# Optimization experiments

Measured on AMD Instinct MI355X. Metric: run time of the kernel, lower is better.

Reference implementation:

```python
import jax, jax.numpy as jnp
import numpy as np

N_NODES = 80000
N_EDGES = 1280000
IN_C, HID_C, OUT_C = 128, 64, 40


def setup_inputs() -> dict:
    key = jax.random.key(0)
    k1, k2, k3, k4 = jax.random.split(key, 4)
    x = jax.random.normal(k1, (N_NODES, IN_C), dtype=jnp.float32)
    edge_index = jax.random.randint(k2, (2, N_EDGES), 0, N_NODES, dtype=jnp.int32)
    W1 = jax.random.normal(k3, (IN_C, HID_C), dtype=jnp.float32) * (1.0 / np.sqrt(IN_C))
    W2 = jax.random.normal(k4, (HID_C, OUT_C), dtype=jnp.float32) * (1.0 / np.sqrt(HID_C))
    return {"x": x, "edge_index": edge_index, "W1": W1, "W2": W2}


def _spmm_add(edge_index, h):
    # adj_t.matmul(h): out[dst] += h[src]  (aggr='add', message = x_j)
    src, dst = edge_index[0], edge_index[1]
    return jax.ops.segment_sum(h[src], dst, num_segments=N_NODES)


def reference(x, edge_index, W1, W2):
    # GCNConv 1: linear (no bias) then add-aggregate SpMM
    h = _spmm_add(edge_index, x @ W1)          # [N, HID]
    h = jax.nn.relu(h)
    # GCNConv 2
    h = _spmm_add(edge_index, h @ W2)          # [N, OUT]
    return jax.nn.log_softmax(h, axis=-1)
```

## Files before the change

### kernel.cpp

```cpp
#include <hip/hip_runtime.h>
#include <hip/hip_bf16.h>
#include <math.h>

#define N_NODES 80000
#define N_EDGES 1280000
#define IN_C 128
#define HID_C 64
#define OUT_C 40

#define KB 313
#define BK_CAP 4600
#define EPT_A 8
#define NBLK_A 313
#define NBLK_G1 625

__device__ __forceinline__ float bf_lo(unsigned u) {
    union { unsigned i; float f; } c; c.i = u << 16; return c.f;
}
__device__ __forceinline__ float bf_hi(unsigned u) {
    union { unsigned i; float f; } c; c.i = u & 0xffff0000u; return c.f;
}
__device__ __forceinline__ unsigned pack_bf2(float a, float b) {
    union { float f; unsigned i; } ca, cb; ca.f = a; cb.f = b;
    unsigned ra = (ca.i + 0x7fffu + ((ca.i >> 16) & 1u)) >> 16;
    unsigned rb = (cb.i + 0x7fffu + ((cb.i >> 16) & 1u)) >> 16;
    return ra | (rb << 16);
}

typedef short v8s __attribute__((ext_vector_type(8)));
typedef float v4f __attribute__((ext_vector_type(4)));
typedef float v2f __attribute__((ext_vector_type(2)));
union U16 { uint4 u; v8s s; };

__device__ __forceinline__ v2f bf2f(unsigned u) {
    return (v2f){bf_lo(u), bf_hi(u)};
}

__global__ void prep_w_kernel(const float* __restrict__ W1, const float* __restrict__ W2,
                              unsigned* __restrict__ w1t, unsigned* __restrict__ w2t,
                              int* __restrict__ bcnt) {
    const int g = blockIdx.x * 256 + threadIdx.x;
    if (g < KB) bcnt[g] = 0;
    {
        const int wcol = g >> 6, kk = g & 63;
        w1t[g] = pack_bf2(W1[(2 * kk) * HID_C + wcol], W1[(2 * kk + 1) * HID_C + wcol]);
    }
    if (g < 1536) {
        const int wcol = g >> 5, kk = g & 31;
        w2t[g] = (wcol < OUT_C)
            ? pack_bf2(W2[(2 * kk) * OUT_C + wcol], W2[(2 * kk + 1) * OUT_C + wcol])
            : 0u;
    }
}

__global__ __launch_bounds__(512) void binA_gemm1_kernel(const int* __restrict__ src,
                                                         const int* __restrict__ dst,
                                                         int* __restrict__ bcnt,
                                                         int* __restrict__ gbuf,
                                                         const float* __restrict__ x,
                                                         const unsigned* __restrict__ w1t,
                                                         unsigned* __restrict__ h1b) {
    if (blockIdx.x >= NBLK_A) {
        const int tid = threadIdx.x;
        const int wave = tid >> 6, lane = tid & 63;
        const int nl = lane & 15, quad = lane >> 4;
        const int node = ((blockIdx.x - NBLK_A) * 8 + wave) * 16 + nl;

        v4f acc[4];
#pragma unroll
        for (int q = 0; q < 4; ++q) acc[q] = (v4f){0.f, 0.f, 0.f, 0.f};

#pragma unroll
        for (int kit = 0; kit < 4; ++kit) {
            const float* xp = x + (size_t)node * IN_C + kit * 32 + quad * 8;
            const float4 lo = *(const float4*)xp;
            const float4 hi = *(const float4*)(xp + 4);
            U16 bu;
            bu.u.x = pack_bf2(lo.x, lo.y); bu.u.y = pack_bf2(lo.z, lo.w);
            bu.u.z = pack_bf2(hi.x, hi.y); bu.u.w = pack_bf2(hi.z, hi.w);
#pragma unroll
            for (int mt = 0; mt < 4; ++mt) {
                U16 au;
                au.u = *(const uint4*)(w1t + ((mt * 16 + nl) * 64 + kit * 16 + quad * 4));
                acc[mt] = __builtin_amdgcn_mfma_f32_16x16x32_bf16(au.s, bu.s, acc[mt], 0, 0, 0);
            }
        }
#pragma unroll
        for (int mt = 0; mt < 4; ++mt) {
            uint2 o;
            o.x = pack_bf2(acc[mt][0], acc[mt][1]);
            o.y = pack_bf2(acc[mt][2], acc[mt][3]);
            *(uint2*)(h1b + (size_t)node * 32 + mt * 8 + quad * 2) = o;
        }
        return;
    }

    __shared__ int lcnt[KB];
    __shared__ int lexcl[KB];
    __shared__ int lbase[KB];
    __shared__ int lcur[KB];
    __shared__ int stage[512 * EPT_A];
    __shared__ int gaddr[512 * EPT_A];
    const int tid = threadIdx.x;

    for (int i = tid; i < KB; i += 512) lcnt[i] = 0;
    __syncthreads();

    const int e0 = blockIdx.x * 512 * EPT_A;
    int my_s[EPT_A], my_b[EPT_A], my_dl[EPT_A];
#pragma unroll
    for (int j = 0; j < EPT_A; ++j) {
        const int e = e0 + j * 512 + tid;
        if (e < N_EDGES) {
            const int d = dst[e];
            my_s[j] = src[e];
            my_b[j] = d >> 8;
            my_dl[j] = d & 255;
            atomicAdd(&lcnt[my_b[j]], 1);
        } else my_b[j] = -1;
    }
    __syncthreads();

    if (tid < KB) lexcl[tid] = lcnt[tid];
    __syncthreads();
    for (int o = 1; o < KB; o <<= 1) {
        int t = (tid < KB && tid >= o) ? lexcl[tid - o] : 0;
        __syncthreads();
        if (tid < KB) lexcl[tid] += t;
        __syncthreads();
    }
    const int total = lexcl[KB - 1];
    if (tid < KB) {
        lexcl[tid] -= lcnt[tid];
        lbase[tid] = (lcnt[tid] > 0) ? atomicAdd(&bcnt[tid], lcnt[tid]) : 0;
        lcur[tid] = 0;
    }
    __syncthreads();

#pragma unroll
    for (int j = 0; j < EPT_A; ++j) {
        if (my_b[j] >= 0) {
            const int b = my_b[j];
            const int r = atomicAdd(&lcur[b], 1);
            const int li = lexcl[b] + r;
            stage[li] = (my_s[j] << 8) | my_dl[j];
            int gp = lbase[b] + r;
            if (gp >= BK_CAP) gp = BK_CAP - 1;
            gaddr[li] = b * BK_CAP + gp;
        }
    }
    __syncthreads();

    for (int i = tid; i < total; i += 512)
        gbuf[gaddr[i]] = stage[i];
}

__global__ __launch_bounds__(512) void binB_kernel(const int* __restrict__ bcnt,
                                                   const int* __restrict__ gbuf,
                                                   int* __restrict__ rp,
                                                   int* __restrict__ col) {
    __shared__ int sc[KB];
    __shared__ int hist[256];
    __shared__ int excl[256];
    __shared__ int cur[256];
    __shared__ int outb[BK_CAP];
    const int b = blockIdx.x;
    const int tid = threadIdx.x;

    if (tid < KB) sc[tid] = min(bcnt[tid], BK_CAP);
    __syncthreads();
    for (int o = 1; o < KB; o <<= 1) {
        int t = (tid < KB && tid >= o) ? sc[tid - o] : 0;
        __syncthreads();
        if (tid < KB) sc[tid] += t;
        __syncthreads();
    }
    const int n = min(bcnt[b], BK_CAP);
    const int cbase = sc[b] - n;
    const int* __restrict__ my = gbuf + (size_t)b * BK_CAP;

    if (tid < 256) hist[tid] = 0;
    __syncthreads();
    for (int i = tid; i < n; i += 512)
        atomicAdd(&hist[my[i] & 255], 1);
    __syncthreads();

    int h = 0;
    if (tid < 256) { h = hist[tid]; excl[tid] = h; }
    __syncthreads();
    for (int o = 1; o < 256; o <<= 1) {
        int t = (tid < 256 && tid >= o) ? excl[tid - o] : 0;
        __syncthreads();
        if (tid < 256) excl[tid] += t;
        __syncthreads();
    }
    if (tid < 256) {
        const int ex = excl[tid] - h;
        cur[tid] = ex;
        const int node = b * 256 + tid;
        if (node <= N_NODES) rp[node] = cbase + ex;
    }
    __syncthreads();

    for (int i = tid; i < n; i += 512) {
        const int pk = my[i];
        const int pos = atomicAdd(&cur[pk & 255], 1);
        outb[pos] = pk >> 8;
    }
    __syncthreads();
    for (int i = tid; i < n; i += 512)
        col[cbase + i] = outb[i];
}

__global__ __launch_bounds__(512) void gather64_g2_kernel(const int* __restrict__ rp,
                                                          const int* __restrict__ col,
                                                          const unsigned* __restrict__ h1b,
                                                          const unsigned* __restrict__ w2t,
                                                          unsigned* __restrict__ h2f) {
    __shared__ int lcol[1536];
    __shared__ unsigned aggLds[16 * 36];
    const int tid = threadIdx.x;
    const int lane = tid & 63;
    const int wave = tid >> 6;
    const int sl = lane & 31;
    const int es = sl >> 3;
    const int cl = sl & 7;
    const int nb = blockIdx.x * 16;

    const int seg_b = rp[nb];
    const int seg_n = min(rp[nb + 16] - seg_b, 1536);
    for (int i = tid; i < seg_n; i += 512) lcol[i] = col[seg_b + i];
    __syncthreads();

    const int nloc = wave * 2 + (lane >> 5);
    const int node = nb + nloc;
    const int b = rp[node], e = rp[node + 1];

    v2f acc[4];
#pragma unroll
    for (int k = 0; k < 4; ++k) acc[k] = (v2f){0.f, 0.f};

    for (int pos = b; __any(pos < e); pos += 32) {
#pragma unroll
        for (int j = 0; j < 8; ++j) {
            const int ei = pos + (j << 2) + es;
            if (ei < e) {
                const int o = ei - seg_b;
                const int s = (o < seg_n) ? lcol[o] : col[ei];
                const uint4 v = *(const uint4*)(h1b + (size_t)s * 32 + cl * 4);
                acc[0] += bf2f(v.x); acc[1] += bf2f(v.y);
                acc[2] += bf2f(v.z); acc[3] += bf2f(v.w);
            }
        }
    }
#pragma unroll
    for (int k = 0; k < 4; ++k) {
        acc[k][0] += __shfl_down(acc[k][0], 16, 64);
        acc[k][1] += __shfl_down(acc[k][1], 16, 64);
    }
#pragma unroll
    for (int k = 0; k < 4; ++k) {
        acc[k][0] += __shfl_down(acc[k][0], 8, 64);
        acc[k][1] += __shfl_down(acc[k][1], 8, 64);
    }

    if (sl < 8) {
        uint4 o;
        o.x = pack_bf2(fmaxf(acc[0][0], 0.f), fmaxf(acc[0][1], 0.f));
        o.y = pack_bf2(fmaxf(acc[1][0], 0.f), fmaxf(acc[1][1], 0.f));
        o.z = pack_bf2(fmaxf(acc[2][0], 0.f), fmaxf(acc[2][1], 0.f));
        o.w = pack_bf2(fmaxf(acc[3][0], 0.f), fmaxf(acc[3][1], 0.f));
        *(uint4*)(aggLds + nloc * 36 + cl * 4) = o;
    }
    __syncthreads();

    if (wave == 0) {
        const int nl = lane & 15, quad = lane >> 4;
        v4f c[3];
#pragma unroll
        for (int q = 0; q < 3; ++q) c[q] = (v4f){0.f, 0.f, 0.f, 0.f};

#pragma unroll
        for (int kit = 0; kit < 2; ++kit) {
            U16 bu;
            bu.u = *(const uint4*)(aggLds + nl * 36 + kit * 16 + quad * 4);
#pragma unroll
            for (int mt = 0; mt < 3; ++mt) {
                U16 au;
                au.u = *(const uint4*)(w2t + ((mt * 16 + nl) * 32 + kit * 16 + quad * 4));
                c[mt] = __builtin_amdgcn_mfma_f32_16x16x32_bf16(au.s, bu.s, c[mt], 0, 0, 0);
            }
        }
        const int node2 = nb + nl;
#pragma unroll
        for (int mt = 0; mt < 3; ++mt) {
            const int idx = mt * 4 + quad;
            if (idx < 10) {
                int u = 0;
                u = __builtin_amdgcn_cvt_pk_fp8_f32(c[mt][0], c[mt][1], u, false);
                u = __builtin_amdgcn_cvt_pk_fp8_f32(c[mt][2], c[mt][3], u, true);
                h2f[(size_t)node2 * 10 + idx] = (unsigned)u;
            }
        }
    }
}

__global__ void gather40_ls_kernel(const int* __restrict__ rp, const int* __restrict__ col,
                                   const unsigned* __restrict__ h2f,
                                   float* __restrict__ out) {
    __shared__ int lcol[1024];
    const int tid = threadIdx.x;
    const int lane = tid & 63;
    const int wave = tid >> 6;
    const int sl = lane & 15;
    const int es = sl / 5;
    const int cl = sl - es * 5;
    const int gbase = lane & 48;
    const int nb = blockIdx.x * 16;

    const int seg_b = rp[nb];
    const int seg_n = min(rp[nb + 16] - seg_b, 1024);
    for (int i = tid; i < seg_n; i += 256) lcol[i] = col[seg_b + i];
    __syncthreads();

    const int node = nb + wave * 4 + (lane >> 4);
    const int b = rp[node], e = rp[node + 1];

    v2f a[4];
#pragma unroll
    for (int k = 0; k < 4; ++k) a[k] = (v2f){0.f, 0.f};

    for (int pos = b; __any(pos < e); pos += 24) {
#pragma unroll
        for (int j = 0; j < 8; ++j) {
            const int ei = pos + j * 3 + es;
            if ((es < 3) && (ei < e)) {
                const int o = ei - seg_b;
                const int s = (o < seg_n) ? lcol[o] : col[ei];
                const uint2 v = *(const uint2*)(h2f + (size_t)s * 10 + cl * 2);
                a[0] += __builtin_amdgcn_cvt_pk_f32_fp8((int)v.x, false);
                a[1] += __builtin_amdgcn_cvt_pk_f32_fp8((int)v.x, true);
                a[2] += __builtin_amdgcn_cvt_pk_f32_fp8((int)v.y, false);
                a[3] += __builtin_amdgcn_cvt_pk_f32_fp8((int)v.y, true);
            }
        }
    }
#pragma unroll
    for (int k = 0; k < 4; ++k) {
#pragma unroll
        for (int h = 0; h < 2; ++h) {
            const float u = __shfl_down(a[k][h], 5, 64);
            const float w = __shfl_down(a[k][h], 10, 64);
            a[k][h] += u + w;
        }
    }

    const bool own = sl < 5;
    float m = -INFINITY;
    if (own) {
#pragma unroll
        for (int k = 0; k < 4; ++k) m = fmaxf(m, fmaxf(a[k][0], a[k][1]));
    }
    const float m0 = __shfl(m, gbase + 0, 64), m1 = __shfl(m, gbase + 1, 64);
    const float m2 = __shfl(m, gbase + 2, 64), m3 = __shfl(m, gbase + 3, 64);
    const float m4 = __shfl(m, gbase + 4, 64);
    const float gm = fmaxf(fmaxf(fmaxf(m0, m1), fmaxf(m2, m3)), m4);

    float s = 0.f;
    if (own) {
#pragma unroll
        for (int k = 0; k < 4; ++k)
            s += __expf(a[k][0] - gm) + __expf(a[k][1] - gm);
    }
    const float s0 = __shfl(s, gbase + 0, 64), s1 = __shfl(s, gbase + 1, 64);
    const float s2 = __shfl(s, gbase + 2, 64), s3 = __shfl(s, gbase + 3, 64);
    const float s4 = __shfl(s, gbase + 4, 64);
    const float ls = __logf(s0 + s1 + s2 + s3 + s4) + gm;

    if (own) {
        float* op = out + (size_t)node * OUT_C + cl * 8;
        *(float4*)op = make_float4(a[0][0] - ls, a[0][1] - ls, a[1][0] - ls, a[1][1] - ls);
        *(float4*)(op + 4) = make_float4(a[2][0] - ls, a[2][1] - ls, a[3][0] - ls, a[3][1] - ls);
    }
}

extern "C" void kernel_launch(void* const* d_in, const int* in_sizes, int n_in,
                              void* d_out, int out_size, void* d_ws, size_t ws_size,
                              hipStream_t stream) {
    const float* x  = (const float*)d_in[0];
    const int* eidx = (const int*)d_in[1];
    const float* W1 = (const float*)d_in[2];
    const float* W2 = (const float*)d_in[3];
    float* out = (float*)d_out;

    const int* src = eidx;
    const int* dst = eidx + N_EDGES;

    unsigned* h1b   = (unsigned*)d_ws;
    unsigned* agg1b = h1b + (size_t)N_NODES * 32;
    unsigned* h2f   = agg1b + (size_t)N_NODES * 32;
    int*      gbuf  = (int*)(h2f + (size_t)N_NODES * 10);
    int*      col   = gbuf + (size_t)KB * BK_CAP;
    int*      rp    = col + N_EDGES;
    int*      bcnt  = rp + (N_NODES + 1);
    unsigned* w1t   = (unsigned*)(bcnt + KB);
    unsigned* w2t   = w1t + 4096;

    prep_w_kernel<<<16, 256, 0, stream>>>(W1, W2, w1t, w2t, bcnt);
    binA_gemm1_kernel<<<NBLK_A + NBLK_G1, 512, 0, stream>>>(src, dst, bcnt, gbuf, x, w1t, h1b);
    binB_kernel<<<KB, 512, 0, stream>>>(bcnt, gbuf, rp, col);

    gather64_g2_kernel<<<N_NODES / 16, 512, 0, stream>>>(rp, col, h1b, w2t, h2f);
    gather40_ls_kernel<<<N_NODES / 16, 256, 0, stream>>>(rp, col, h2f, out);
}
```

Baseline: 177.4 us.

## Replace two-pass bucket CSR build with degree histogram, scan, and atomic scatter

Drops the LDS-staged bucket binning (binA/binB) used to build the CSR. It now counts per-node degrees with global atomics, scans them to get row pointers, and scatters each edge's source into col through a per-node atomic cursor. This removes the intermediate bucket buffer, its capacity clamp, and the second read/sort pass, at the cost of many contended global atomics. Rows are no longer in a deterministic order, and the scatter adds one more kernel launch.

```diff
diff --git a/kernel.cpp b/kernel.cpp
--- a/kernel.cpp
+++ b/kernel.cpp
@@ -9,9 +9,7 @@
 #define OUT_C 40
 
 #define KB 313
-#define BK_CAP 4600
-#define EPT_A 8
-#define NBLK_A 313
+#define HB 160
 #define NBLK_G1 625
 
 __device__ __forceinline__ float bf_lo(unsigned u) {
@@ -38,10 +36,11 @@
 
 __global__ void prep_w_kernel(const float* __restrict__ W1, const float* __restrict__ W2,
                               unsigned* __restrict__ w1t, unsigned* __restrict__ w2t,
-                              int* __restrict__ bcnt) {
+                              int* __restrict__ deg, int* __restrict__ bsum) {
     const int g = blockIdx.x * 256 + threadIdx.x;
-    if (g < KB) bcnt[g] = 0;
-    {
+    if (g < N_NODES) deg[g] = 0;
+    if (g < KB) bsum[g] = 0;
+    if (g < 4096) {
         const int wcol = g >> 6, kk = g & 63;
         w1t[g] = pack_bf2(W1[(2 * kk) * HID_C + wcol], W1[(2 * kk + 1) * HID_C + wcol]);
     }
@@ -53,18 +52,17 @@
     }
 }
 
-__global__ __launch_bounds__(512) void binA_gemm1_kernel(const int* __restrict__ src,
-                                                         const int* __restrict__ dst,
-                                                         int* __restrict__ bcnt,
-                                                         int* __restrict__ gbuf,
+__global__ __launch_bounds__(512) void hist_gemm1_kernel(const int* __restrict__ dst,
+                                                         int* __restrict__ deg,
+                                                         int* __restrict__ bsum,
                                                          const float* __restrict__ x,
                                                          const unsigned* __restrict__ w1t,
                                                          unsigned* __restrict__ h1b) {
-    if (blockIdx.x >= NBLK_A) {
+    if (blockIdx.x >= HB) {
         const int tid = threadIdx.x;
         const int wave = tid >> 6, lane = tid & 63;
         const int nl = lane & 15, quad = lane >> 4;
-        const int node = ((blockIdx.x - NBLK_A) * 8 + wave) * 16 + nl;
+        const int node = ((blockIdx.x - HB) * 8 + wave) * 16 + nl;
 
         v4f acc[4];
 #pragma unroll
@@ -95,121 +93,71 @@
         return;
     }
 
-    __shared__ int lcnt[KB];
-    __shared__ int lexcl[KB];
-    __shared__ int lbase[KB];
-    __shared__ int lcur[KB];
-    __shared__ int stage[512 * EPT_A];
-    __shared__ int gaddr[512 * EPT_A];
+    __shared__ int lh[KB];
     const int tid = threadIdx.x;
-
-    for (int i = tid; i < KB; i += 512) lcnt[i] = 0;
-    __syncthreads();
-
-    const int e0 = blockIdx.x * 512 * EPT_A;
-    int my_s[EPT_A], my_b[EPT_A], my_dl[EPT_A];
-#pragma unroll
-    for (int j = 0; j < EPT_A; ++j) {
-        const int e = e0 + j * 512 + tid;
-        if (e < N_EDGES) {
-            const int d = dst[e];
-            my_s[j] = src[e];
-            my_b[j] = d >> 8;
-            my_dl[j] = d & 255;
-            atomicAdd(&lcnt[my_b[j]], 1);
-        } else my_b[j] = -1;
-    }
-    __syncthreads();
-
-    if (tid < KB) lexcl[tid] = lcnt[tid];
+    for (int i = tid; i < KB; i += 512) lh[i] = 0;
+    __syncthreads();
+
+    const int4* __restrict__ d4 = (const int4*)dst;
+    for (int i = blockIdx.x * 512 + tid; i < N_EDGES / 4; i += HB * 512) {
+        const int4 d = d4[i];
+        atomicAdd(&deg[d.x], 1); atomicAdd(&lh[d.x >> 8], 1);
+        atomicAdd(&deg[d.y], 1); atomicAdd(&lh[d.y >> 8], 1);
+        atomicAdd(&deg[d.z], 1); atomicAdd(&lh[d.z >> 8], 1);
+        atomicAdd(&deg[d.w], 1); atomicAdd(&lh[d.w >> 8], 1);
+    }
+    __syncthreads();
+    for (int i = tid; i < KB; i += 512)
+        if (lh[i]) atomicAdd(&bsum[i], lh[i]);
+}
+
+__global__ __launch_bounds__(512) void scan_fin_kernel(const int* __restrict__ deg,
+                                                       const int* __restrict__ bsum,
+                                                       int* __restrict__ rp,
+                                                       int* __restrict__ cur) {
+    __shared__ int sb[KB];
+    __shared__ int sd[256];
+    const int b = blockIdx.x, tid = threadIdx.x;
+
+    if (tid < KB) sb[tid] = bsum[tid];
     __syncthreads();
     for (int o = 1; o < KB; o <<= 1) {
-        int t = (tid < KB && tid >= o) ? lexcl[tid - o] : 0;
+        int t = (tid < KB && tid >= o) ? sb[tid - o] : 0;
         __syncthreads();
-        if (tid < KB) lexcl[tid] += t;
+        if (tid < KB) sb[tid] += t;
         __syncthreads();
     }
-    const int total = lexcl[KB - 1];
-    if (tid < KB) {
-        lexcl[tid] -= lcnt[tid];
-        lbase[tid] = (lcnt[tid] > 0) ? atomicAdd(&bcnt[tid], lcnt[tid]) : 0;
-        lcur[tid] = 0;
-    }
-    __syncthreads();
-
-#pragma unroll
-    for (int j = 0; j < EPT_A; ++j) {
-        if (my_b[j] >= 0) {
-            const int b = my_b[j];
-            const int r = atomicAdd(&lcur[b], 1);
-            const int li = lexcl[b] + r;
-            stage[li] = (my_s[j] << 8) | my_dl[j];
-            int gp = lbase[b] + r;
-            if (gp >= BK_CAP) gp = BK_CAP - 1;
-            gaddr[li] = b * BK_CAP + gp;
-        }
-    }
-    __syncthreads();
-
-    for (int i = tid; i < total; i += 512)
-        gbuf[gaddr[i]] = stage[i];
-}
-
-__global__ __launch_bounds__(512) void binB_kernel(const int* __restrict__ bcnt,
-                                                   const int* __restrict__ gbuf,
-                                                   int* __restrict__ rp,
-                                                   int* __restrict__ col) {
-    __shared__ int sc[KB];
-    __shared__ int hist[256];
-    __shared__ int excl[256];
-    __shared__ int cur[256];
-    __shared__ int outb[BK_CAP];
-    const int b = blockIdx.x;
-    const int tid = threadIdx.x;
-
-    if (tid < KB) sc[tid] = min(bcnt[tid], BK_CAP);
-    __syncthreads();
-    for (int o = 1; o < KB; o <<= 1) {
-        int t = (tid < KB && tid >= o) ? sc[tid - o] : 0;
+    const int boff = (b == 0) ? 0 : sb[b - 1];
+
+    const int node = b * 256 + tid;
+    int d = 0;
+    if (tid < 256 && node < N_NODES) d = deg[node];
+    if (tid < 256) sd[tid] = d;
+    __syncthreads();
+    for (int o = 1; o < 256; o <<= 1) {
+        int t = (tid < 256 && tid >= o) ? sd[tid - o] : 0;
         __syncthreads();
-        if (tid < KB) sc[tid] += t;
+        if (tid < 256) sd[tid] += t;
         __syncthreads();
     }
-    const int n = min(bcnt[b], BK_CAP);
-    const int cbase = sc[b] - n;
-    const int* __restrict__ my = gbuf + (size_t)b * BK_CAP;
-
-    if (tid < 256) hist[tid] = 0;
-    __syncthreads();
-    for (int i = tid; i < n; i += 512)
-        atomicAdd(&hist[my[i] & 255], 1);
-    __syncthreads();
-
-    int h = 0;
-    if (tid < 256) { h = hist[tid]; excl[tid] = h; }
-    __syncthreads();
-    for (int o = 1; o < 256; o <<= 1) {
-        int t = (tid < 256 && tid >= o) ? excl[tid - o] : 0;
-        __syncthreads();
-        if (tid < 256) excl[tid] += t;
-        __syncthreads();
-    }
-    if (tid < 256) {
-        const int ex = excl[tid] - h;
-        cur[tid] = ex;
-        const int node = b * 256 + tid;
-        if (node <= N_NODES) rp[node] = cbase + ex;
-    }
-    __syncthreads();
-
-    for (int i = tid; i < n; i += 512) {
-        const int pk = my[i];
-        const int pos = atomicAdd(&cur[pk & 255], 1);
-        outb[pos] = pk >> 8;
-    }
-    __syncthreads();
-    for (int i = tid; i < n; i += 512)
-        col[cbase + i] = outb[i];
+    if (tid < 256 && node <= N_NODES) {
+        const int v = boff + sd[tid] - d;
+        rp[node] = v;
+        if (node < N_NODES) cur[node] = v;
+    }
+}
+
+__global__ __launch_bounds__(512) void scatter_kernel(const int* __restrict__ src,
+                                                      const int* __restrict__ dst,
+                                                      int* __restrict__ cur,
+                                                      int* __restrict__ col) {
+    const int i = blockIdx.x * 512 + threadIdx.x;
+    const int4 s = ((const int4*)src)[i];
+    const int4 d = ((const int4*)dst)[i];
+    col[atomicAdd(&cur[d.x], 1)] = s.x;
+    col[atomicAdd(&cur[d.y], 1)] = s.y;
+    col[atomicAdd(&cur[d.z], 1)] = s.z;
+    col[atomicAdd(&cur[d.w], 1)] = s.w;
 }
 
 __global__ __launch_bounds__(512) void gather64_g2_kernel(const int* __restrict__ rp,
@@ -396,19 +344,20 @@
     const int* src = eidx;
     const int* dst = eidx + N_EDGES;
 
-    unsigned* h1b   = (unsigned*)d_ws;
-    unsigned* agg1b = h1b + (size_t)N_NODES * 32;
-    unsigned* h2f   = agg1b + (size_t)N_NODES * 32;
-    int*      gbuf  = (int*)(h2f + (size_t)N_NODES * 10);
-    int*      col   = gbuf + (size_t)KB * BK_CAP;
-    int*      rp    = col + N_EDGES;
-    int*      bcnt  = rp + (N_NODES + 1);
-    unsigned* w1t   = (unsigned*)(bcnt + KB);
-    unsigned* w2t   = w1t + 4096;
-
-    prep_w_kernel<<<16, 256, 0, stream>>>(W1, W2, w1t, w2t, bcnt);
-    binA_gemm1_kernel<<<NBLK_A + NBLK_G1, 512, 0, stream>>>(src, dst, bcnt, gbuf, x, w1t, h1b);
-    binB_kernel<<<KB, 512, 0, stream>>>(bcnt, gbuf, rp, col);
+    unsigned* h1b  = (unsigned*)d_ws;
+    unsigned* h2f  = h1b + (size_t)N_NODES * 32;
+    int*      col  = (int*)(h2f + (size_t)N_NODES * 10);
+    int*      rp   = col + N_EDGES;
+    int*      deg  = rp + 80004;
+    int*      cur  = deg + N_NODES;
+    int*      bsum = cur + N_NODES;
+    unsigned* w1t  = (unsigned*)(bsum + 316);
+    unsigned* w2t  = w1t + 4096;
+
+    prep_w_kernel<<<313, 256, 0, stream>>>(W1, W2, w1t, w2t, deg, bsum);
+    hist_gemm1_kernel<<<HB + NBLK_G1, 512, 0, stream>>>(dst, deg, bsum, x, w1t, h1b);
+    scan_fin_kernel<<<KB, 512, 0, stream>>>(deg, bsum, rp, cur);
+    scatter_kernel<<<N_EDGES / 4 / 512, 512, 0, stream>>>(src, dst, cur, col);
 
     gather64_g2_kernel<<<N_NODES / 16, 512, 0, stream>>>(rp, col, h1b, w2t, h2f);
     gather40_ls_kernel<<<N_NODES / 16, 256, 0, stream>>>(rp, col, h2f, out);
```

Result: slower. 293.1 us (+65.2%).
